# Kernel tuning notes

Hardware: AMD Instinct MI355X
Metric: run time of the kernel (lower is better)

The kernel has to match this reference:

```python
import jax, jax.numpy as jnp
import numpy as np
import math

N_EMBD = 1024
N_HEAD = 16
B, T = 2, 2048


def new_gelu(x):
    # GPT-2 tanh-approx GELU (matches torch module exactly)
    return 0.5 * x * (1.0 + jnp.tanh(jnp.sqrt(2.0 / jnp.pi) * (x + 0.044715 * x ** 3)))


def layer_norm(x, w, b, eps=1e-5):
    mu = jnp.mean(x, axis=-1, keepdims=True)
    var = jnp.var(x, axis=-1, keepdims=True)
    return (x - mu) * jax.lax.rsqrt(var + eps) * w + b


def setup_inputs() -> dict:
    key = jax.random.key(0)
    ks = jax.random.split(key, 8)
    C = N_EMBD
    s = 0.02
    return {
        "x": jax.random.normal(ks[0], (B, T, C), dtype=jnp.float32),
        "ln1_w": jnp.ones((C,), jnp.float32),
        "ln1_b": jnp.zeros((C,), jnp.float32),
        "attn_w": s * jax.random.normal(ks[1], (C, 3 * C), jnp.float32),
        "attn_b": jnp.zeros((3 * C,), jnp.float32),
        "attn_proj_w": s * jax.random.normal(ks[2], (C, C), jnp.float32),
        "attn_proj_b": jnp.zeros((C,), jnp.float32),
        "ln2_w": jnp.ones((C,), jnp.float32),
        "ln2_b": jnp.zeros((C,), jnp.float32),
        "fc_w": s * jax.random.normal(ks[3], (C, 4 * C), jnp.float32),
        "fc_b": jnp.zeros((4 * C,), jnp.float32),
        "mlp_proj_w": s * jax.random.normal(ks[4], (4 * C, C), jnp.float32),
        "mlp_proj_b": jnp.zeros((C,), jnp.float32),
    }


def block_forward(x, ln1_w, ln1_b, attn_w, attn_b, attn_proj_w, attn_proj_b,
                  ln2_w, ln2_b, fc_w, fc_b, mlp_proj_w, mlp_proj_b):
    Bm, Tm, C = x.shape
    H = N_HEAD
    D = C // H
    # --- self attention (pre-LN) ---
    h = layer_norm(x, ln1_w, ln1_b)
    qkv = h @ attn_w + attn_b  # [B,T,3C]
    q, k, v = jnp.split(qkv, 3, axis=-1)
    q = q.reshape(Bm, Tm, H, D).transpose(0, 2, 1, 3)  # [B,H,T,D]
    k = k.reshape(Bm, Tm, H, D).transpose(0, 2, 1, 3)
    v = v.reshape(Bm, Tm, H, D).transpose(0, 2, 1, 3)
    att = jnp.einsum('bhqd,bhkd->bhqk', q, k) * (1.0 / math.sqrt(D))
    att = jax.nn.softmax(att, axis=-1)  # NOTE: no causal mask in source
    y = jnp.einsum('bhqk,bhkd->bhqd', att, v)
    y = y.transpose(0, 2, 1, 3).reshape(Bm, Tm, C)
    x = x + (y @ attn_proj_w + attn_proj_b)
    # --- MLP ---
    h = layer_norm(x, ln2_w, ln2_b)
    h = new_gelu(h @ fc_w + fc_b)
    x = x + (h @ mlp_proj_w + mlp_proj_b)
    return x


def reference(x, ln1_w, ln1_b, attn_w, attn_b, attn_proj_w, attn_proj_b,
              ln2_w, ln2_b, fc_w, fc_b, mlp_proj_w, mlp_proj_b):
    return block_forward(x, ln1_w, ln1_b, attn_w, attn_b, attn_proj_w, attn_proj_b,
                         ln2_w, ln2_b, fc_w, fc_b, mlp_proj_w, mlp_proj_b)
```

## Files before the change

kernel.cpp:

```cpp
#include <hip/hip_runtime.h>

typedef __attribute__((ext_vector_type(4)))  float  f32x4;
typedef __attribute__((ext_vector_type(16))) float  f32x16;
typedef __attribute__((ext_vector_type(8)))  short  s16x8;
typedef __attribute__((ext_vector_type(4)))  short  s16x4;
typedef __attribute__((ext_vector_type(4)))  unsigned u32x4;
typedef __attribute__((ext_vector_type(2)))  unsigned u32x2;
typedef __attribute__((ext_vector_type(2)))  int    i32x2;

__device__ __forceinline__ short f2bf(float f) {
    unsigned u = __builtin_bit_cast(unsigned, f);
    u += 0x7fff + ((u >> 16) & 1);
    return (short)(u >> 16);
}

__device__ __forceinline__ void load_lds16(const void* g, void* l) {
    __builtin_amdgcn_global_load_lds(
        (const __attribute__((address_space(1))) unsigned int*)g,
        (__attribute__((address_space(3))) unsigned int*)l, 16, 0, 0);
}

__device__ __forceinline__ float tsum32(const f32x16& a, const f32x16& b) {
    float u[16];
#pragma unroll
    for (int i = 0; i < 16; i++) u[i] = a[i] + b[i];
#pragma unroll
    for (int i = 0; i < 8; i++) u[i] += u[i + 8];
#pragma unroll
    for (int i = 0; i < 4; i++) u[i] += u[i + 4];
    return (u[0] + u[2]) + (u[1] + u[3]);
}

__global__ __launch_bounds__(256) void transpose_cast(const float* __restrict__ W,
                                                      short* __restrict__ Wt,
                                                      int K, int N) {
    __shared__ float t[32][33];
    int n0 = blockIdx.x * 32, k0 = blockIdx.y * 32;
    int tx = threadIdx.x & 31, ty = threadIdx.x >> 5;
#pragma unroll
    for (int i = 0; i < 4; i++)
        t[ty + 8 * i][tx] = W[(size_t)(k0 + ty + 8 * i) * N + n0 + tx];
    __syncthreads();
#pragma unroll
    for (int i = 0; i < 4; i++)
        Wt[(size_t)(n0 + ty + 8 * i) * K + k0 + tx] = f2bf(t[tx][ty + 8 * i]);
}

__global__ __launch_bounds__(256) void ln_kernel(const float* __restrict__ x,
                                                 const float* __restrict__ w,
                                                 const float* __restrict__ b,
                                                 short* __restrict__ out) {
    int row = blockIdx.x;
    int tid = threadIdx.x;
    const float4 v = ((const float4*)(x + (size_t)row * 1024))[tid];
    float s  = v.x + v.y + v.z + v.w;
    float ss = v.x * v.x + v.y * v.y + v.z * v.z + v.w * v.w;
#pragma unroll
    for (int o = 32; o > 0; o >>= 1) {
        s  += __shfl_down(s, o);
        ss += __shfl_down(ss, o);
    }
    __shared__ float rs[4], rq[4];
    int wave = tid >> 6, lane = tid & 63;
    if (lane == 0) { rs[wave] = s; rq[wave] = ss; }
    __syncthreads();
    float tot = rs[0] + rs[1] + rs[2] + rs[3];
    float tq  = rq[0] + rq[1] + rq[2] + rq[3];
    float mu   = tot * (1.f / 1024.f);
    float var  = tq * (1.f / 1024.f) - mu * mu;
    float rstd = rsqrtf(var + 1e-5f);
    const float4 wv = ((const float4*)w)[tid];
    const float4 bv = ((const float4*)b)[tid];
    s16x4 o;
    o[0] = f2bf((v.x - mu) * rstd * wv.x + bv.x);
    o[1] = f2bf((v.y - mu) * rstd * wv.y + bv.y);
    o[2] = f2bf((v.z - mu) * rstd * wv.z + bv.z);
    o[3] = f2bf((v.w - mu) * rstd * wv.w + bv.w);
    ((s16x4*)(out + (size_t)row * 1024))[tid] = o;
}

__device__ __forceinline__ void xcd_remap(int& bx, int& by) {
    int gx = gridDim.x, gy = gridDim.y;
    int hwid = blockIdx.y * gx + blockIdx.x;
    int xcd = hwid & 7, rank = hwid >> 3;
    int pan = gx >> 3;
    bx = xcd * pan + rank / gy;
    by = rank % gy;
}

template <typename OUT_T, bool GELU, bool RES, bool SCALE_Q, bool VSPLIT>
__global__ __launch_bounds__(256) void gemm_bt(const short* __restrict__ A,
                                               const short* __restrict__ Bt,
                                               const float* __restrict__ bias,
                                               const float* __restrict__ res,
                                               OUT_T* __restrict__ C,
                                               short* __restrict__ vtg,
                                               int M, int N, int K) {
    __shared__ __align__(16) short As[2][128 * 32];
    __shared__ __align__(16) short Bs[2][128 * 32];
    int tid = threadIdx.x;
    int bx, by;
    xcd_remap(bx, by);
    int m0 = by * 128, n0 = bx * 128;
    int wave = tid >> 6, lane = tid & 63;
    int wr = wave >> 1, wc = wave & 1;
    int g = lane >> 4, q = lane & 15;
    f32x4 acc[4][4] = {};
    const short* Ab = A + (size_t)m0 * K;
    const short* Bb = Bt + (size_t)n0 * K;
    int srow = tid >> 2;
    int scol = (tid & 3) * 8;
    auto stage = [&](int bi, int k0) {
        load_lds16(Ab + (size_t)srow * K + k0 + scol, &As[bi][tid * 8]);
        load_lds16(Ab + (size_t)(srow + 64) * K + k0 + scol, &As[bi][2048 + tid * 8]);
        load_lds16(Bb + (size_t)srow * K + k0 + scol, &Bs[bi][tid * 8]);
        load_lds16(Bb + (size_t)(srow + 64) * K + k0 + scol, &Bs[bi][2048 + tid * 8]);
    };
    int nk = K >> 5;
    stage(0, 0);
    __syncthreads();
    for (int kk = 0; kk < nk; ++kk) {
        int cur = kk & 1;
        if (kk + 1 < nk) stage(cur ^ 1, (kk + 1) << 5);
        s16x8 a[4], bf[4];
#pragma unroll
        for (int mi = 0; mi < 4; mi++)
            a[mi] = *(const s16x8*)(&As[cur][(wr * 64 + mi * 16 + q) * 32 + g * 8]);
#pragma unroll
        for (int ni = 0; ni < 4; ni++)
            bf[ni] = *(const s16x8*)(&Bs[cur][(wc * 64 + ni * 16 + q) * 32 + g * 8]);
#pragma unroll
        for (int mi = 0; mi < 4; mi++)
#pragma unroll
            for (int ni = 0; ni < 4; ni++)
                acc[mi][ni] = __builtin_amdgcn_mfma_f32_16x16x32_bf16(a[mi], bf[ni], acc[mi][ni], 0, 0, 0);
        __syncthreads();
    }
#pragma unroll
    for (int mi = 0; mi < 4; mi++) {
#pragma unroll
        for (int ni = 0; ni < 4; ni++) {
            int row = m0 + wr * 64 + mi * 16 + g * 4;
            int col = n0 + wc * 64 + ni * 16 + q;
            float bb = bias[col];
            if (VSPLIT && col >= 2048) {
                int d = col & 63;
                int bh2 = ((row >> 11) << 4) + ((col - 2048) >> 6);
                s16x4 o;
#pragma unroll
                for (int r = 0; r < 4; r++) o[r] = f2bf(acc[mi][ni][r] + bb);
                *(s16x4*)&vtg[((size_t)bh2 * 64 + d) * 2048 + (row & 2047)] = o;
            } else {
#pragma unroll
                for (int r = 0; r < 4; r++) {
                    float v = acc[mi][ni][r] + bb;
                    if (RES) v += res[(size_t)(row + r) * N + col];
                    if (GELU) {
                        float aa = 0.7978845608028654f * (v + 0.044715f * v * v * v);
                        float th = 1.f - 2.f / (__expf(2.f * aa) + 1.f);
                        v = 0.5f * v * (1.f + th);
                    }
                    if (SCALE_Q && col < 1024) v *= 0.18033688011112042f;
                    if constexpr (sizeof(OUT_T) == 2)
                        C[(size_t)(row + r) * N + col] = f2bf(v);
                    else
                        C[(size_t)(row + r) * N + col] = v;
                }
            }
        }
    }
}

__global__ __launch_bounds__(256) void gemm_bt_sk(const short* __restrict__ A,
                                                  const short* __restrict__ Bt,
                                                  float* __restrict__ part,
                                                  int M, int N, int K, int Klen) {
    __shared__ __align__(16) short As[2][128 * 32];
    __shared__ __align__(16) short Bs[2][128 * 32];
    int tid = threadIdx.x;
    int bx, by;
    xcd_remap(bx, by);
    int m0 = by * 128, n0 = bx * 128;
    int kz = blockIdx.z;
    int wave = tid >> 6, lane = tid & 63;
    int wr = wave >> 1, wc = wave & 1;
    int g = lane >> 4, q = lane & 15;
    f32x4 acc[4][4] = {};
    const short* Ab = A + (size_t)m0 * K;
    const short* Bb = Bt + (size_t)n0 * K;
    int srow = tid >> 2;
    int scol = (tid & 3) * 8;
    auto stage = [&](int bi, int k0) {
        load_lds16(Ab + (size_t)srow * K + k0 + scol, &As[bi][tid * 8]);
        load_lds16(Ab + (size_t)(srow + 64) * K + k0 + scol, &As[bi][2048 + tid * 8]);
        load_lds16(Bb + (size_t)srow * K + k0 + scol, &Bs[bi][tid * 8]);
        load_lds16(Bb + (size_t)(srow + 64) * K + k0 + scol, &Bs[bi][2048 + tid * 8]);
    };
    int kbase = kz * Klen;
    int nk = Klen >> 5;
    stage(0, kbase);
    __syncthreads();
    for (int kk = 0; kk < nk; ++kk) {
        int cur = kk & 1;
        if (kk + 1 < nk) stage(cur ^ 1, kbase + ((kk + 1) << 5));
        s16x8 a[4], bf[4];
#pragma unroll
        for (int mi = 0; mi < 4; mi++)
            a[mi] = *(const s16x8*)(&As[cur][(wr * 64 + mi * 16 + q) * 32 + g * 8]);
#pragma unroll
        for (int ni = 0; ni < 4; ni++)
            bf[ni] = *(const s16x8*)(&Bs[cur][(wc * 64 + ni * 16 + q) * 32 + g * 8]);
#pragma unroll
        for (int mi = 0; mi < 4; mi++)
#pragma unroll
            for (int ni = 0; ni < 4; ni++)
                acc[mi][ni] = __builtin_amdgcn_mfma_f32_16x16x32_bf16(a[mi], bf[ni], acc[mi][ni], 0, 0, 0);
        __syncthreads();
    }
    float* pb = part + (size_t)kz * M * N;
#pragma unroll
    for (int mi = 0; mi < 4; mi++) {
#pragma unroll
        for (int ni = 0; ni < 4; ni++) {
            int row = m0 + wr * 64 + mi * 16 + g * 4;
            int col = n0 + wc * 64 + ni * 16 + q;
#pragma unroll
            for (int r = 0; r < 4; r++)
                pb[(size_t)(row + r) * N + col] = acc[mi][ni][r];
        }
    }
}

template <int SK>
__global__ __launch_bounds__(256) void reduce_sk(const float* __restrict__ part,
                                                 const float* __restrict__ bias,
                                                 const float* __restrict__ res,
                                                 float* __restrict__ out,
                                                 int MN, int N) {
    int tot = MN >> 2;
    int nb4 = (N >> 2) - 1;
    for (int i = blockIdx.x * 256 + threadIdx.x; i < tot; i += gridDim.x * 256) {
        float4 s = ((const float4*)part)[i];
#pragma unroll
        for (int k = 1; k < SK; k++) {
            float4 p = ((const float4*)(part + (size_t)k * MN))[i];
            s.x += p.x; s.y += p.y; s.z += p.z; s.w += p.w;
        }
        float4 bv = ((const float4*)bias)[i & nb4];
        float4 rv = ((const float4*)res)[i];
        float4 o;
        o.x = s.x + bv.x + rv.x;
        o.y = s.y + bv.y + rv.y;
        o.z = s.z + bv.z + rv.z;
        o.w = s.w + bv.w + rv.w;
        ((float4*)out)[i] = o;
    }
}

__global__ __launch_bounds__(64, 2) void attn_kernel(const short* __restrict__ qkv,
                                                     const short* __restrict__ Vtg,
                                                     short* __restrict__ y) {
    const int T = 2048, C3 = 3072;
    int wg = blockIdx.x;
    int mapped = (wg & 7) * 256 + (wg >> 3);
    int bh = mapped >> 6, qt = mapped & 63;
    int b = bh >> 4, h = bh & 15;
    int lane = threadIdx.x;
    int ql = lane & 31, hi = lane >> 5;
    const short* base = qkv + (size_t)b * T * C3;

    int qrow = qt * 32 + ql;
    const short* qp = base + (size_t)qrow * C3 + h * 64;
    s16x8 qf[4];
#pragma unroll
    for (int s = 0; s < 4; s++)
        qf[s] = *(const s16x8*)(qp + ((2 * s + hi) << 3));

    __shared__ __align__(16) short Ks[2][64 * 64];

    const short* kbase = base + 1024 + h * 64 + (size_t)(lane >> 3) * C3
                       + (((lane & 7) ^ ((lane >> 3) & 7)) << 3);
    const short* vbase = Vtg + ((size_t)bh * 64 + ql) * T + (hi << 3);

    auto stageK = [&](int bi, int t) {
#pragma unroll
        for (int i = 0; i < 8; i++)
            load_lds16(kbase + (size_t)(t * 64 + 8 * i) * C3, &Ks[bi][i * 512]);
    };
    auto loadV = [&](s16x8* V, int t) {
        const short* p = vbase + t * 64;
#pragma unroll
        for (int s = 0; s < 4; s++) {
            V[s]     = *(const s16x8*)(p + 16 * s);
            V[4 + s] = *(const s16x8*)(p + (size_t)32 * T + 16 * s);
        }
    };

    float lst = 0.f;
    f32x16 accY0 = {}, accY1 = {};
    int swz = ql & 7;
    s16x8 va[8], vb[8];

    stageK(0, 0);
    loadV(va, 0);

    auto tile = [&](int bi, const s16x8* VC, s16x8* VN, int t) {
        if (t < 31) {
            stageK(bi ^ 1, t + 1);
            loadV(VN, t + 1);
            asm volatile("s_waitcnt vmcnt(16)" ::: "memory");
        } else {
            asm volatile("s_waitcnt vmcnt(8)" ::: "memory");
        }
        __builtin_amdgcn_sched_barrier(0);
        f32x16 s0 = {}, s1 = {};
        const short* kb0 = &Ks[bi][ql * 64];
        const short* kb1 = &Ks[bi][(32 + ql) * 64];
        __builtin_amdgcn_s_setprio(1);
#pragma unroll
        for (int s = 0; s < 4; s++) {
            int c = ((2 * s + hi) ^ swz) << 3;
            s16x8 k0 = *(const s16x8*)(kb0 + c);
            s16x8 k1 = *(const s16x8*)(kb1 + c);
            s0 = __builtin_amdgcn_mfma_f32_32x32x16_bf16(k0, qf[s], s0, 0, 0, 0);
            s1 = __builtin_amdgcn_mfma_f32_32x32x16_bf16(k1, qf[s], s1, 0, 0, 0);
        }
        __builtin_amdgcn_s_setprio(0);
#pragma unroll
        for (int r = 0; r < 16; r++) s0[r] = exp2f(s0[r]);
#pragma unroll
        for (int r = 0; r < 16; r++) s1[r] = exp2f(s1[r]);
        float ps = tsum32(s0, s1);
        ps += __shfl_xor(ps, 32);
        lst += ps;
        s16x8 pb[4];
#pragma unroll
        for (int s = 0; s < 4; s++) {
            int tt = (s & 1) * 8;
            unsigned lo0, lo1, hi0, hi1;
            if (s < 2) {
                asm("v_cvt_pk_bf16_f32 %0, %1, %2" : "=v"(lo0) : "v"(s0[tt + 0]), "v"(s0[tt + 1]));
                asm("v_cvt_pk_bf16_f32 %0, %1, %2" : "=v"(lo1) : "v"(s0[tt + 2]), "v"(s0[tt + 3]));
                asm("v_cvt_pk_bf16_f32 %0, %1, %2" : "=v"(hi0) : "v"(s0[tt + 4]), "v"(s0[tt + 5]));
                asm("v_cvt_pk_bf16_f32 %0, %1, %2" : "=v"(hi1) : "v"(s0[tt + 6]), "v"(s0[tt + 7]));
            } else {
                asm("v_cvt_pk_bf16_f32 %0, %1, %2" : "=v"(lo0) : "v"(s1[tt + 0]), "v"(s1[tt + 1]));
                asm("v_cvt_pk_bf16_f32 %0, %1, %2" : "=v"(lo1) : "v"(s1[tt + 2]), "v"(s1[tt + 3]));
                asm("v_cvt_pk_bf16_f32 %0, %1, %2" : "=v"(hi0) : "v"(s1[tt + 4]), "v"(s1[tt + 5]));
                asm("v_cvt_pk_bf16_f32 %0, %1, %2" : "=v"(hi1) : "v"(s1[tt + 6]), "v"(s1[tt + 7]));
            }
            i32x2 r0 = __builtin_amdgcn_permlane32_swap((int)hi0, (int)lo0, false, false);
            i32x2 r1 = __builtin_amdgcn_permlane32_swap((int)hi1, (int)lo1, false, false);
            u32x4 w;
            w[0] = (unsigned)r0[1]; w[1] = (unsigned)r1[1];
            w[2] = (unsigned)r0[0]; w[3] = (unsigned)r1[0];
            pb[s] = __builtin_bit_cast(s16x8, w);
        }
        __builtin_amdgcn_s_setprio(1);
#pragma unroll
        for (int s = 0; s < 4; s++) {
            accY0 = __builtin_amdgcn_mfma_f32_32x32x16_bf16(VC[s], pb[s], accY0, 0, 0, 0);
            accY1 = __builtin_amdgcn_mfma_f32_32x32x16_bf16(VC[4 + s], pb[s], accY1, 0, 0, 0);
        }
        __builtin_amdgcn_s_setprio(0);
    };

    for (int t = 0; t < 32; t += 2) {
        tile(0, va, vb, t);
        tile(1, vb, va, t + 1);
    }

    float linv = 1.f / lst;
    short* yrow = y + ((size_t)b * T + qrow) * 1024 + h * 64;
#pragma unroll
    for (int r = 0; r < 4; r++) {
        unsigned w0, w1, w2, w3;
        float a0 = accY0[4 * r] * linv, a1 = accY0[4 * r + 1] * linv;
        float a2 = accY0[4 * r + 2] * linv, a3 = accY0[4 * r + 3] * linv;
        float b0 = accY1[4 * r] * linv, b1 = accY1[4 * r + 1] * linv;
        float b2 = accY1[4 * r + 2] * linv, b3 = accY1[4 * r + 3] * linv;
        asm("v_cvt_pk_bf16_f32 %0, %1, %2" : "=v"(w0) : "v"(a0), "v"(a1));
        asm("v_cvt_pk_bf16_f32 %0, %1, %2" : "=v"(w1) : "v"(a2), "v"(a3));
        asm("v_cvt_pk_bf16_f32 %0, %1, %2" : "=v"(w2) : "v"(b0), "v"(b1));
        asm("v_cvt_pk_bf16_f32 %0, %1, %2" : "=v"(w3) : "v"(b2), "v"(b3));
        u32x2 p0; p0[0] = w0; p0[1] = w1;
        u32x2 p1; p1[0] = w2; p1[1] = w3;
        *(u32x2*)(yrow + 8 * r + 4 * hi)      = p0;
        *(u32x2*)(yrow + 32 + 8 * r + 4 * hi) = p1;
    }
}

extern "C" void kernel_launch(void* const* d_in, const int* in_sizes, int n_in,
                              void* d_out, int out_size, void* d_ws, size_t ws_size,
                              hipStream_t stream) {
    const float* x           = (const float*)d_in[0];
    const float* ln1_w       = (const float*)d_in[1];
    const float* ln1_b       = (const float*)d_in[2];
    const float* attn_w      = (const float*)d_in[3];
    const float* attn_b      = (const float*)d_in[4];
    const float* attn_proj_w = (const float*)d_in[5];
    const float* attn_proj_b = (const float*)d_in[6];
    const float* ln2_w       = (const float*)d_in[7];
    const float* ln2_b       = (const float*)d_in[8];
    const float* fc_w        = (const float*)d_in[9];
    const float* fc_b        = (const float*)d_in[10];
    const float* mlp_proj_w  = (const float*)d_in[11];
    const float* mlp_proj_b  = (const float*)d_in[12];

    const int M = 4096;

    size_t off = 0;
    char* wsb = (char*)d_ws;
    auto alloc = [&](size_t bytes) {
        void* p = wsb + off;
        off += (bytes + 255) & ~(size_t)255;
        return p;
    };
    short* wt_attn  = (short*)alloc(3072ull * 1024 * 2);
    short* wt_proj  = (short*)alloc(1024ull * 1024 * 2);
    short* wt_fc    = (short*)alloc(4096ull * 1024 * 2);
    short* wt_mproj = (short*)alloc(1024ull * 4096 * 2);
    short* h1       = (short*)alloc((size_t)M * 1024 * 2);
    short* qkvb     = (short*)alloc((size_t)M * 3072 * 2);
    short* yb       = (short*)alloc((size_t)M * 1024 * 2);
    float* x1       = (float*)alloc((size_t)M * 1024 * 4);
    short* vtg      = (short*)alloc((size_t)M * 1024 * 2);
    short* h2       = qkvb;

    size_t base_off = off;
    int SK = 0;
    if (ws_size >= base_off + 4ull * M * 1024 * 4) SK = 4;
    else if (ws_size >= base_off + 2ull * M * 1024 * 4) SK = 2;
    float* part = (float*)(wsb + base_off);

    transpose_cast<<<dim3(3072 / 32, 1024 / 32), 256, 0, stream>>>(attn_w, wt_attn, 1024, 3072);
    transpose_cast<<<dim3(1024 / 32, 1024 / 32), 256, 0, stream>>>(attn_proj_w, wt_proj, 1024, 1024);
    transpose_cast<<<dim3(4096 / 32, 1024 / 32), 256, 0, stream>>>(fc_w, wt_fc, 1024, 4096);
    transpose_cast<<<dim3(1024 / 32, 4096 / 32), 256, 0, stream>>>(mlp_proj_w, wt_mproj, 4096, 1024);

    ln_kernel<<<M, 256, 0, stream>>>(x, ln1_w, ln1_b, h1);
    gemm_bt<short, false, false, true, true><<<dim3(3072 / 128, M / 128), 256, 0, stream>>>(
        h1, wt_attn, attn_b, nullptr, qkvb, vtg, M, 3072, 1024);
    attn_kernel<<<2048, 64, 0, stream>>>(qkvb, vtg, yb);
    gemm_bt<float, false, true, false, false><<<dim3(1024 / 128, M / 128), 256, 0, stream>>>(
        yb, wt_proj, attn_proj_b, x, x1, nullptr, M, 1024, 1024);
    ln_kernel<<<M, 256, 0, stream>>>(x1, ln2_w, ln2_b, h1);
    gemm_bt<short, true, false, false, false><<<dim3(4096 / 128, M / 128), 256, 0, stream>>>(
        h1, wt_fc, fc_b, nullptr, h2, nullptr, M, 4096, 1024);

    if (SK == 4) {
        gemm_bt_sk<<<dim3(1024 / 128, M / 128, 4), 256, 0, stream>>>(
            h2, wt_mproj, part, M, 1024, 4096, 1024);
        reduce_sk<4><<<2048, 256, 0, stream>>>(part, mlp_proj_b, x1, (float*)d_out, M * 1024, 1024);
    } else if (SK == 2) {
        gemm_bt_sk<<<dim3(1024 / 128, M / 128, 2), 256, 0, stream>>>(
            h2, wt_mproj, part, M, 1024, 4096, 2048);
        reduce_sk<2><<<2048, 256, 0, stream>>>(part, mlp_proj_b, x1, (float*)d_out, M * 1024, 1024);
    } else {
        gemm_bt<float, false, true, false, false><<<dim3(1024 / 128, M / 128), 256, 0, stream>>>(
            h2, wt_mproj, mlp_proj_b, x1, (float*)d_out, nullptr, M, 1024, 4096);
    }
}
```

Measured before the change: 306.8 us.

## Share K/V tiles in LDS across two waves per attention workgroup

The attention kernel now runs two waves per workgroup, each handling 32 query rows, so one workgroup covers 64 queries. Both K and V tiles are staged cooperatively into swizzled double-buffered LDS and shared by the two waves, where before each single-wave block loaded V straight into registers. The aim is to halve global K/V traffic per query and free the registers that held V. In exchange it adds a __syncthreads per tile and replaces the hand-tuned vmcnt waits with barrier-based pipelining, which may expose latency.

After: 292.3 us. 4.7% less time.

```diff
diff --git a/kernel.cpp b/kernel.cpp
--- a/kernel.cpp
+++ b/kernel.cpp
@@ -257,19 +257,19 @@
     }
 }
 
-__global__ __launch_bounds__(64, 2) void attn_kernel(const short* __restrict__ qkv,
-                                                     const short* __restrict__ Vtg,
-                                                     short* __restrict__ y) {
+__global__ __launch_bounds__(128) void attn_kernel(const short* __restrict__ qkv,
+                                                   const short* __restrict__ Vtg,
+                                                   short* __restrict__ y) {
     const int T = 2048, C3 = 3072;
     int wg = blockIdx.x;
-    int mapped = (wg & 7) * 256 + (wg >> 3);
-    int bh = mapped >> 6, qt = mapped & 63;
+    int mapped = (wg & 7) * 128 + (wg >> 3);
+    int bh = mapped >> 5, qt = mapped & 31;
     int b = bh >> 4, h = bh & 15;
-    int lane = threadIdx.x;
+    int tid = threadIdx.x, lane = tid & 63, wave = tid >> 6;
     int ql = lane & 31, hi = lane >> 5;
     const short* base = qkv + (size_t)b * T * C3;
 
-    int qrow = qt * 32 + ql;
+    int qrow = qt * 64 + wave * 32 + ql;
     const short* qp = base + (size_t)qrow * C3 + h * 64;
     s16x8 qf[4];
 #pragma unroll
@@ -277,45 +277,36 @@
         qf[s] = *(const s16x8*)(qp + ((2 * s + hi) << 3));
 
     __shared__ __align__(16) short Ks[2][64 * 64];
-
-    const short* kbase = base + 1024 + h * 64 + (size_t)(lane >> 3) * C3
-                       + (((lane & 7) ^ ((lane >> 3) & 7)) << 3);
-    const short* vbase = Vtg + ((size_t)bh * 64 + ql) * T + (hi << 3);
-
-    auto stageK = [&](int bi, int t) {
-#pragma unroll
-        for (int i = 0; i < 8; i++)
-            load_lds16(kbase + (size_t)(t * 64 + 8 * i) * C3, &Ks[bi][i * 512]);
-    };
-    auto loadV = [&](s16x8* V, int t) {
-        const short* p = vbase + t * 64;
-#pragma unroll
-        for (int s = 0; s < 4; s++) {
-            V[s]     = *(const s16x8*)(p + 16 * s);
-            V[4 + s] = *(const s16x8*)(p + (size_t)32 * T + 16 * s);
+    __shared__ __align__(16) short Vs[2][64 * 64];
+
+    int srow = tid >> 3, sc8 = tid & 7;
+    const short* kp = base + 1024 + h * 64 + (size_t)srow * C3 + ((sc8 ^ (srow & 7)) << 3);
+    const short* vp = Vtg + ((size_t)bh * 64 + srow) * T + ((sc8 ^ (srow & 7)) << 3);
+
+    auto stage = [&](int bi) {
+#pragma unroll
+        for (int i = 0; i < 4; i++) {
+            load_lds16(kp + (size_t)(16 * i) * C3, &Ks[bi][i * 1024 + tid * 8]);
+            load_lds16(vp + (size_t)(16 * i) * T,  &Vs[bi][i * 1024 + tid * 8]);
         }
     };
 
     float lst = 0.f;
     f32x16 accY0 = {}, accY1 = {};
     int swz = ql & 7;
-    s16x8 va[8], vb[8];
-
-    stageK(0, 0);
-    loadV(va, 0);
-
-    auto tile = [&](int bi, const s16x8* VC, s16x8* VN, int t) {
+
+    stage(0);
+    for (int t = 0; t < 32; ++t) {
+        int cur = t & 1;
+        __syncthreads();
         if (t < 31) {
-            stageK(bi ^ 1, t + 1);
-            loadV(VN, t + 1);
-            asm volatile("s_waitcnt vmcnt(16)" ::: "memory");
-        } else {
-            asm volatile("s_waitcnt vmcnt(8)" ::: "memory");
-        }
-        __builtin_amdgcn_sched_barrier(0);
+            kp += 64 * C3;
+            vp += 64;
+            stage(cur ^ 1);
+        }
         f32x16 s0 = {}, s1 = {};
-        const short* kb0 = &Ks[bi][ql * 64];
-        const short* kb1 = &Ks[bi][(32 + ql) * 64];
+        const short* kb0 = &Ks[cur][ql * 64];
+        const short* kb1 = &Ks[cur][(32 + ql) * 64];
         __builtin_amdgcn_s_setprio(1);
 #pragma unroll
         for (int s = 0; s < 4; s++) {
@@ -356,20 +347,19 @@
             w[2] = (unsigned)r0[0]; w[3] = (unsigned)r1[0];
             pb[s] = __builtin_bit_cast(s16x8, w);
         }
+        const short* vb0 = &Vs[cur][ql * 64];
+        const short* vb1 = &Vs[cur][(32 + ql) * 64];
         __builtin_amdgcn_s_setprio(1);
 #pragma unroll
         for (int s = 0; s < 4; s++) {
-            accY0 = __builtin_amdgcn_mfma_f32_32x32x16_bf16(VC[s], pb[s], accY0, 0, 0, 0);
-            accY1 = __builtin_amdgcn_mfma_f32_32x32x16_bf16(VC[4 + s], pb[s], accY1, 0, 0, 0);
+            int c = ((2 * s + hi) ^ swz) << 3;
+            s16x8 v0 = *(const s16x8*)(vb0 + c);
+            s16x8 v1 = *(const s16x8*)(vb1 + c);
+            accY0 = __builtin_amdgcn_mfma_f32_32x32x16_bf16(v0, pb[s], accY0, 0, 0, 0);
+            accY1 = __builtin_amdgcn_mfma_f32_32x32x16_bf16(v1, pb[s], accY1, 0, 0, 0);
         }
         __builtin_amdgcn_s_setprio(0);
-    };
-
-    for (int t = 0; t < 32; t += 2) {
-        tile(0, va, vb, t);
-        tile(1, vb, va, t + 1);
-    }
-
+    }
     float linv = 1.f / lst;
     short* yrow = y + ((size_t)b * T + qrow) * 1024 + h * 64;
 #pragma unroll
@@ -441,7 +431,7 @@
     ln_kernel<<<M, 256, 0, stream>>>(x, ln1_w, ln1_b, h1);
     gemm_bt<short, false, false, true, true><<<dim3(3072 / 128, M / 128), 256, 0, stream>>>(
         h1, wt_attn, attn_b, nullptr, qkvb, vtg, M, 3072, 1024);
-    attn_kernel<<<2048, 64, 0, stream>>>(qkvb, vtg, yb);
+    attn_kernel<<<1024, 128, 0, stream>>>(qkvb, vtg, yb);
     gemm_bt<float, false, true, false, false><<<dim3(1024 / 128, M / 128), 256, 0, stream>>>(
         yb, wt_proj, attn_proj_b, x, x1, nullptr, M, 1024, 1024);
     ln_kernel<<<M, 256, 0, stream>>>(x1, ln2_w, ln2_b, h1);
```
